# Kernel optimization log

Measured on AMD Instinct MI355X. Metric: run time of the kernel, lower is better.

Reference implementation:

```python
import jax, jax.numpy as jnp
import numpy as np

N_NODES = 100000
N_EDGES = 1600000
N_GRAPHS = 512
IN_DIM, HID, GOUT, SCAL = 256, 128, 64, 2


def setup_inputs() -> dict:
    key = jax.random.key(0)
    ks = jax.random.split(key, 12)
    x = jax.random.normal(ks[0], (N_NODES, IN_DIM), dtype=jnp.float32)
    edge_index = jax.random.randint(ks[1], (2, N_EDGES), 0, N_NODES, dtype=jnp.int64)
    batch = jnp.sort(jax.random.randint(ks[2], (N_NODES,), 0, N_GRAPHS, dtype=jnp.int64))
    scalars = jax.random.normal(ks[3], (N_GRAPHS, SCAL), dtype=jnp.float32)
    def lin(k, fan_in, fan_out):
        s = 1.0 / np.sqrt(fan_in)
        kw, kb = jax.random.split(k)
        W = jax.random.uniform(kw, (fan_in, fan_out), minval=-s, maxval=s, dtype=jnp.float32)
        b = jax.random.uniform(kb, (fan_out,), minval=-s, maxval=s, dtype=jnp.float32)
        return W, b
    W1, b1 = lin(ks[4], IN_DIM, HID)
    W2, b2 = lin(ks[5], HID, GOUT)
    W3, b3 = lin(ks[6], GOUT + SCAL, HID)
    W4, b4 = lin(ks[7], HID, 1)
    return {"x": x, "edge_index": edge_index, "batch": batch, "scalars": scalars,
            "W1": W1, "b1": b1, "W2": W2, "b2": b2,
            "W3": W3, "b3": b3, "W4": W4, "b4": b4}


def gcn_conv(x, W, b, src, dst, num_nodes):
    # PyG GCNConv: h = x @ W; add self-loops; norm = d^-1/2[src] * d^-1/2[dst]
    # with deg = in-degree (on dst) + 1 (self-loop); scatter-add into dst.
    h = x @ W  # [N, F]
    deg = jax.ops.segment_sum(jnp.ones((src.shape[0],), h.dtype), dst,
                              num_segments=num_nodes) + 1.0
    dinv = jax.lax.rsqrt(deg)  # [N]
    norm = dinv[src] * dinv[dst]  # [E]
    agg = jax.ops.segment_sum(h[src] * norm[:, None], dst, num_segments=num_nodes)
    agg = agg + h * (dinv * dinv)[:, None]  # self-loop contribution
    return agg + b


def global_mean_pool(x, batch, num_graphs):
    s = jax.ops.segment_sum(x, batch, num_segments=num_graphs)
    cnt = jax.ops.segment_sum(jnp.ones((x.shape[0],), x.dtype), batch,
                              num_segments=num_graphs)
    return s / jnp.maximum(cnt, 1.0)[:, None]


def reference(x, edge_index, batch, scalars, W1, b1, W2, b2, W3, b3, W4, b4):
    src, dst = edge_index[0], edge_index[1]
    h = jax.nn.relu(gcn_conv(x, W1, b1, src, dst, N_NODES))
    h = gcn_conv(h, W2, b2, src, dst, N_NODES)
    emb = global_mean_pool(h, batch, N_GRAPHS)  # [G, GOUT]
    combined = jnp.concatenate([emb, scalars], axis=1)  # [G, GOUT+SCAL]
    out = jax.nn.sigmoid(jax.nn.relu(combined @ W3 + b3) @ W4 + b4)
    return out.reshape(-1, 1)
```

## Files before the change

### kernel.cpp

```cpp
#include <hip/hip_runtime.h>

#define NN 100000
#define NE 1600000
#define NG 512
#define NPARTS 500
#define PW 200
#define NCHUNKS 128
#define CE 12500
#define NCNT (NPARTS * NCHUNKS)

typedef unsigned int uint;
typedef unsigned short ushort;
typedef __bf16 bf16x8 __attribute__((ext_vector_type(8)));
typedef float f32x4 __attribute__((ext_vector_type(4)));

__device__ inline uint f2bf2(float a, float b) {
  uint ua = __float_as_uint(a), ub = __float_as_uint(b);
  ua += 0x7fff + ((ua >> 16) & 1);
  ub += 0x7fff + ((ub >> 16) & 1);
  return (ua >> 16) | (ub & 0xffff0000u);
}
__device__ inline ushort f2bf(float f) {
  uint u = __float_as_uint(f);
  u += 0x7fff + ((u >> 16) & 1);
  return (ushort)(u >> 16);
}
__device__ inline float2 bf2f(uint v) {
  float2 r;
  r.x = __uint_as_float(v << 16);
  r.y = __uint_as_float(v & 0xffff0000u);
  return r;
}
__device__ inline uint relu2(uint u) {
  uint lo = (u & 0x8000u) ? 0u : (u & 0xFFFFu);
  uint hi = (u & 0x80000000u) ? 0u : (u & 0xFFFF0000u);
  return lo | hi;
}

__global__ __launch_bounds__(256) void transpose_w2(const float* __restrict__ W1, uint* __restrict__ w1t,
                                                    const float* __restrict__ W2, uint* __restrict__ w2t) {
  __shared__ float col[256];
  int b = blockIdx.x, k = threadIdx.x;
  const float* W; uint* Wt; int K, N, n;
  if (b < 128) { W = W1; Wt = w1t; K = 256; N = 128; n = b; }
  else         { W = W2; Wt = w2t; K = 128; N = 64;  n = b - 128; }
  if (k < K) col[k] = W[(size_t)k * N + n];
  __syncthreads();
  if (k < K / 2) Wt[(size_t)n * (K / 2) + k] = f2bf2(col[2 * k], col[2 * k + 1]);
}

__global__ __launch_bounds__(256) void bucket_count(const int* __restrict__ dst,
                                                    int* __restrict__ cnt) {
  __shared__ int h[NPARTS];
  int t = threadIdx.x, c = blockIdx.x;
  for (int i = t; i < NPARTS; i += 256) h[i] = 0;
  __syncthreads();
  int beg = c * CE;
  for (int j = t; j < CE; j += 256) atomicAdd(&h[dst[beg + j] / PW], 1);
  __syncthreads();
  for (int i = t; i < NPARTS; i += 256) cnt[i * NCHUNKS + c] = h[i];
}

__global__ void scan1(const int* __restrict__ in, int* __restrict__ out,
                      int* __restrict__ bsum, int n) {
  __shared__ int s[256];
  int t = threadIdx.x;
  int i = blockIdx.x * 256 + t;
  int v = (i < n) ? in[i] : 0;
  s[t] = v;
  __syncthreads();
  for (int off = 1; off < 256; off <<= 1) {
    int add = (t >= off) ? s[t - off] : 0;
    __syncthreads();
    s[t] += add;
    __syncthreads();
  }
  if (i < n) out[i] = s[t] - v;
  if (t == 255) bsum[blockIdx.x] = s[255];
}

__global__ void scan2(int* __restrict__ bsum, int nb) {
  __shared__ int s[512];
  int t = threadIdx.x;
  int v = (t < nb) ? bsum[t] : 0;
  s[t] = v;
  __syncthreads();
  for (int off = 1; off < 512; off <<= 1) {
    int add = (t >= off) ? s[t - off] : 0;
    __syncthreads();
    s[t] += add;
    __syncthreads();
  }
  if (t < nb) bsum[t] = s[t] - v;
}

__global__ void scan3(int* __restrict__ out, const int* __restrict__ bsum, int n) {
  int i = blockIdx.x * 256 + threadIdx.x;
  if (i < n) out[i] += bsum[blockIdx.x];
}

__global__ __launch_bounds__(256) void bucket_scatter(const int* __restrict__ src,
                                                      const int* __restrict__ dst,
                                                      const int* __restrict__ off,
                                                      uint* __restrict__ pk) {
  __shared__ int cur[NPARTS];
  int t = threadIdx.x, c = blockIdx.x;
  for (int i = t; i < NPARTS; i += 256) cur[i] = off[i * NCHUNKS + c];
  __syncthreads();
  int beg = c * CE;
  for (int j = t; j < CE; j += 256) {
    int d = dst[beg + j];
    int p = d / PW;
    int pos = atomicAdd(&cur[p], 1);
    pk[pos] = (uint)src[beg + j] | ((uint)(d - p * PW) << 17);
  }
}

__global__ __launch_bounds__(256) void csr_finalize(const uint* __restrict__ pk,
                                                    const int* __restrict__ off,
                                                    int* __restrict__ row_off,
                                                    float* __restrict__ dinv,
                                                    int* __restrict__ csr) {
  __shared__ int hist[PW];
  __shared__ int cur[PW];
  __shared__ int s[256];
  int p = blockIdx.x, t = threadIdx.x;
  int base = off[p * NCHUNKS];
  int endp = (p == NPARTS - 1) ? NE : off[(p + 1) * NCHUNKS];
  if (t < PW) hist[t] = 0;
  __syncthreads();
  for (int j = base + t; j < endp; j += 256) atomicAdd(&hist[pk[j] >> 17], 1);
  __syncthreads();
  int v = (t < PW) ? hist[t] : 0;
  s[t] = v;
  __syncthreads();
  for (int o = 1; o < 256; o <<= 1) {
    int add = (t >= o) ? s[t - o] : 0;
    __syncthreads();
    s[t] += add;
    __syncthreads();
  }
  if (t < PW) {
    int excl = base + (s[t] - v);
    int node = p * PW + t;
    row_off[node] = excl;
    dinv[node]    = rsqrtf((float)v + 1.0f);
    cur[t] = excl;
  }
  if (p == NPARTS - 1 && t == 0) row_off[NN] = NE;
  __syncthreads();
  for (int j = base + t; j < endp; j += 256) {
    uint e = pk[j];
    int pos = atomicAdd(&cur[e >> 17], 1);
    csr[pos] = (int)(e & 0x1FFFFu);
  }
}

template<int BM, int BN, int WM, int A_BF16, int RELU>
__global__ __launch_bounds__(256) void mfma_gemm(const void* __restrict__ Av,
                                                 const uint* __restrict__ Bt,
                                                 const float* __restrict__ dinv,
                                                 ushort* __restrict__ Cb,
                                                 int M, int K, int N) {
  constexpr int BK = 32;
  constexpr int AU = BM * BK / 8;
  constexpr int BU = BN * BK / 8;
  __shared__ __align__(16) char smem[BM * BK * 2 + BN * BK * 2];
  char* Asm = smem;
  char* Bsm = smem + BM * BK * 2;

  const int tid  = threadIdx.x;
  const int wid  = tid >> 6;
  const int lane = tid & 63;
  const int wm   = wid % WM;
  const int wn   = wid / WM;
  const int blockRow = blockIdx.x * BM;
  const int l15  = lane & 15;
  const int lk   = lane >> 4;

  f32x4 acc[4][4];
#pragma unroll
  for (int i = 0; i < 4; ++i)
#pragma unroll
    for (int j = 0; j < 4; ++j) acc[i][j] = (f32x4){0.f, 0.f, 0.f, 0.f};

  for (int kk = 0; kk < K; kk += BK) {
#pragma unroll
    for (int i = 0; i < AU / 256; ++i) {
      int u = tid + i * 256;
      int row = u >> 2, oct = u & 3;
      int grow = blockRow + row;
      uint4 v = make_uint4(0, 0, 0, 0);
      if (grow < M) {
        if (A_BF16) {
          const uint* A = (const uint*)Av;
          v = *reinterpret_cast<const uint4*>(A + (size_t)grow * (K / 2) + (kk >> 1) + oct * 4);
          if (RELU) { v.x = relu2(v.x); v.y = relu2(v.y); v.z = relu2(v.z); v.w = relu2(v.w); }
        } else {
          const float* A = (const float*)Av;
          const float4* ptr = reinterpret_cast<const float4*>(A + (size_t)grow * K + kk + oct * 8);
          float4 f0 = ptr[0], f1 = ptr[1];
          v.x = f2bf2(f0.x, f0.y); v.y = f2bf2(f0.z, f0.w);
          v.z = f2bf2(f1.x, f1.y); v.w = f2bf2(f1.z, f1.w);
        }
      }
      int byte = (row * 64 + oct * 16) ^ ((row & 7) << 4);
      *reinterpret_cast<uint4*>(Asm + byte) = v;
    }
#pragma unroll
    for (int i = 0; i < BU / 256; ++i) {
      int u = tid + i * 256;
      int n = u >> 2, oct = u & 3;
      uint4 v = *reinterpret_cast<const uint4*>(Bt + (size_t)n * (K / 2) + (kk >> 1) + oct * 4);
      int byte = (n * 64 + oct * 16) ^ ((n & 7) << 4);
      *reinterpret_cast<uint4*>(Bsm + byte) = v;
    }
    __syncthreads();

    bf16x8 af[4], bfr[4];
#pragma unroll
    for (int mt = 0; mt < 4; ++mt) {
      int row = wm * 64 + mt * 16 + l15;
      int byte = (row * 64 + (lk << 4)) ^ ((row & 7) << 4);
      af[mt] = __builtin_bit_cast(bf16x8, *reinterpret_cast<uint4*>(Asm + byte));
    }
#pragma unroll
    for (int nt = 0; nt < 4; ++nt) {
      int n = wn * 64 + nt * 16 + l15;
      int byte = (n * 64 + (lk << 4)) ^ ((n & 7) << 4);
      bfr[nt] = __builtin_bit_cast(bf16x8, *reinterpret_cast<uint4*>(Bsm + byte));
    }
#pragma unroll
    for (int mt = 0; mt < 4; ++mt)
#pragma unroll
      for (int nt = 0; nt < 4; ++nt)
        acc[mt][nt] = __builtin_amdgcn_mfma_f32_16x16x32_bf16(af[mt], bfr[nt], acc[mt][nt], 0, 0, 0);
    __syncthreads();
  }

#pragma unroll
  for (int mt = 0; mt < 4; ++mt) {
    int rbase = blockRow + wm * 64 + mt * 16 + lk * 4;
#pragma unroll
    for (int j = 0; j < 4; ++j) {
      int grow = rbase + j;
      if (grow < M) {
        float d = dinv[grow];
#pragma unroll
        for (int nt = 0; nt < 4; ++nt) {
          int gcol = wn * 64 + nt * 16 + l15;
          Cb[(size_t)grow * N + gcol] = f2bf(acc[mt][nt][j] * d);
        }
      }
    }
  }
}

__global__ __launch_bounds__(256) void agg_csr_f128_v2(const uint4* __restrict__ hs,
                                                       const float* __restrict__ dinv,
                                                       const float* __restrict__ bias,
                                                       const int* __restrict__ row_off,
                                                       const int* __restrict__ csr,
                                                       uint4* __restrict__ outb, int N) {
  int node = blockIdx.x * 4 + (threadIdx.x >> 6);
  if (node >= N) return;
  int lane = threadIdx.x & 63;
  int sl = lane >> 4;
  int c4 = lane & 15;
  int beg = row_off[node], end = row_off[node + 1];
  float a0=0,a1=0,a2=0,a3=0,a4=0,a5=0,a6=0,a7=0;
  int j = beg;
  for (; j + 16 <= end; j += 16) {
    int s0 = csr[j + sl];
    int s1 = csr[j + 4 + sl];
    int s2 = csr[j + 8 + sl];
    int s3 = csr[j + 12 + sl];
    uint4 v0 = hs[(size_t)s0 * 16 + c4];
    uint4 v1 = hs[(size_t)s1 * 16 + c4];
    uint4 v2 = hs[(size_t)s2 * 16 + c4];
    uint4 v3 = hs[(size_t)s3 * 16 + c4];
    float2 f;
    f = bf2f(v0.x); a0+=f.x; a1+=f.y;  f = bf2f(v0.y); a2+=f.x; a3+=f.y;
    f = bf2f(v0.z); a4+=f.x; a5+=f.y;  f = bf2f(v0.w); a6+=f.x; a7+=f.y;
    f = bf2f(v1.x); a0+=f.x; a1+=f.y;  f = bf2f(v1.y); a2+=f.x; a3+=f.y;
    f = bf2f(v1.z); a4+=f.x; a5+=f.y;  f = bf2f(v1.w); a6+=f.x; a7+=f.y;
    f = bf2f(v2.x); a0+=f.x; a1+=f.y;  f = bf2f(v2.y); a2+=f.x; a3+=f.y;
    f = bf2f(v2.z); a4+=f.x; a5+=f.y;  f = bf2f(v2.w); a6+=f.x; a7+=f.y;
    f = bf2f(v3.x); a0+=f.x; a1+=f.y;  f = bf2f(v3.y); a2+=f.x; a3+=f.y;
    f = bf2f(v3.z); a4+=f.x; a5+=f.y;  f = bf2f(v3.w); a6+=f.x; a7+=f.y;
  }
  for (; j + 4 <= end; j += 4) {
    int s0 = csr[j + sl];
    uint4 v0 = hs[(size_t)s0 * 16 + c4];
    float2 f;
    f = bf2f(v0.x); a0+=f.x; a1+=f.y;  f = bf2f(v0.y); a2+=f.x; a3+=f.y;
    f = bf2f(v0.z); a4+=f.x; a5+=f.y;  f = bf2f(v0.w); a6+=f.x; a7+=f.y;
  }
  if (j + sl < end) {
    int s0 = csr[j + sl];
    uint4 v0 = hs[(size_t)s0 * 16 + c4];
    float2 f;
    f = bf2f(v0.x); a0+=f.x; a1+=f.y;  f = bf2f(v0.y); a2+=f.x; a3+=f.y;
    f = bf2f(v0.z); a4+=f.x; a5+=f.y;  f = bf2f(v0.w); a6+=f.x; a7+=f.y;
  }
  a0 += __shfl_xor(a0, 16); a1 += __shfl_xor(a1, 16); a2 += __shfl_xor(a2, 16); a3 += __shfl_xor(a3, 16);
  a4 += __shfl_xor(a4, 16); a5 += __shfl_xor(a5, 16); a6 += __shfl_xor(a6, 16); a7 += __shfl_xor(a7, 16);
  a0 += __shfl_xor(a0, 32); a1 += __shfl_xor(a1, 32); a2 += __shfl_xor(a2, 32); a3 += __shfl_xor(a3, 32);
  a4 += __shfl_xor(a4, 32); a5 += __shfl_xor(a5, 32); a6 += __shfl_xor(a6, 32); a7 += __shfl_xor(a7, 32);
  if (sl == 0) {
    uint4 v = hs[(size_t)node * 16 + c4];
    float2 f;
    f = bf2f(v.x); a0+=f.x; a1+=f.y;  f = bf2f(v.y); a2+=f.x; a3+=f.y;
    f = bf2f(v.z); a4+=f.x; a5+=f.y;  f = bf2f(v.w); a6+=f.x; a7+=f.y;
    float d = dinv[node];
    const float4* bp = reinterpret_cast<const float4*>(bias);
    float4 b0 = bp[c4 * 2], b1 = bp[c4 * 2 + 1];
    uint4 o;
    o.x = f2bf2(fmaf(a0, d, b0.x), fmaf(a1, d, b0.y));
    o.y = f2bf2(fmaf(a2, d, b0.z), fmaf(a3, d, b0.w));
    o.z = f2bf2(fmaf(a4, d, b1.x), fmaf(a5, d, b1.y));
    o.w = f2bf2(fmaf(a6, d, b1.z), fmaf(a7, d, b1.w));
    outb[(size_t)node * 16 + c4] = o;
  }
}

__global__ __launch_bounds__(256) void agg_csr_f64_v2(const uint4* __restrict__ hs,
                                                      const float* __restrict__ dinv,
                                                      const int* __restrict__ row_off,
                                                      const int* __restrict__ csr,
                                                      float* __restrict__ out, int N) {
  int node = blockIdx.x * 4 + (threadIdx.x >> 6);
  if (node >= N) return;
  int lane = threadIdx.x & 63;
  int sl = lane >> 3;
  int c4 = lane & 7;
  int beg = row_off[node], end = row_off[node + 1];
  float a0=0,a1=0,a2=0,a3=0,a4=0,a5=0,a6=0,a7=0;
  int j = beg;
  for (; j + 16 <= end; j += 16) {
    int s0 = csr[j + sl];
    int s1 = csr[j + 8 + sl];
    uint4 v0 = hs[(size_t)s0 * 8 + c4];
    uint4 v1 = hs[(size_t)s1 * 8 + c4];
    float2 f;
    f = bf2f(v0.x); a0+=f.x; a1+=f.y;  f = bf2f(v0.y); a2+=f.x; a3+=f.y;
    f = bf2f(v0.z); a4+=f.x; a5+=f.y;  f = bf2f(v0.w); a6+=f.x; a7+=f.y;
    f = bf2f(v1.x); a0+=f.x; a1+=f.y;  f = bf2f(v1.y); a2+=f.x; a3+=f.y;
    f = bf2f(v1.z); a4+=f.x; a5+=f.y;  f = bf2f(v1.w); a6+=f.x; a7+=f.y;
  }
  for (; j + 8 <= end; j += 8) {
    int s0 = csr[j + sl];
    uint4 v0 = hs[(size_t)s0 * 8 + c4];
    float2 f;
    f = bf2f(v0.x); a0+=f.x; a1+=f.y;  f = bf2f(v0.y); a2+=f.x; a3+=f.y;
    f = bf2f(v0.z); a4+=f.x; a5+=f.y;  f = bf2f(v0.w); a6+=f.x; a7+=f.y;
  }
  if (j + sl < end) {
    int s0 = csr[j + sl];
    uint4 v0 = hs[(size_t)s0 * 8 + c4];
    float2 f;
    f = bf2f(v0.x); a0+=f.x; a1+=f.y;  f = bf2f(v0.y); a2+=f.x; a3+=f.y;
    f = bf2f(v0.z); a4+=f.x; a5+=f.y;  f = bf2f(v0.w); a6+=f.x; a7+=f.y;
  }
  a0 += __shfl_xor(a0, 8);  a1 += __shfl_xor(a1, 8);  a2 += __shfl_xor(a2, 8);  a3 += __shfl_xor(a3, 8);
  a4 += __shfl_xor(a4, 8);  a5 += __shfl_xor(a5, 8);  a6 += __shfl_xor(a6, 8);  a7 += __shfl_xor(a7, 8);
  a0 += __shfl_xor(a0, 16); a1 += __shfl_xor(a1, 16); a2 += __shfl_xor(a2, 16); a3 += __shfl_xor(a3, 16);
  a4 += __shfl_xor(a4, 16); a5 += __shfl_xor(a5, 16); a6 += __shfl_xor(a6, 16); a7 += __shfl_xor(a7, 16);
  a0 += __shfl_xor(a0, 32); a1 += __shfl_xor(a1, 32); a2 += __shfl_xor(a2, 32); a3 += __shfl_xor(a3, 32);
  a4 += __shfl_xor(a4, 32); a5 += __shfl_xor(a5, 32); a6 += __shfl_xor(a6, 32); a7 += __shfl_xor(a7, 32);
  if (sl == 0) {
    uint4 v = hs[(size_t)node * 8 + c4];
    float2 f;
    f = bf2f(v.x); a0+=f.x; a1+=f.y;  f = bf2f(v.y); a2+=f.x; a3+=f.y;
    f = bf2f(v.z); a4+=f.x; a5+=f.y;  f = bf2f(v.w); a6+=f.x; a7+=f.y;
    float d = dinv[node];
    float4 o0 = make_float4(a0 * d, a1 * d, a2 * d, a3 * d);
    float4 o1 = make_float4(a4 * d, a5 * d, a6 * d, a7 * d);
    float4* op = reinterpret_cast<float4*>(out + (size_t)node * 64 + c4 * 8);
    op[0] = o0;
    op[1] = o1;
  }
}

__global__ __launch_bounds__(256) void pool_graph(const float* __restrict__ h,
                                                  const int* __restrict__ batch,
                                                  const float* __restrict__ scalars,
                                                  float* __restrict__ emb66, int N) {
  int g = blockIdx.x;
  int t = threadIdx.x;
  int col = t & 63, rr = t >> 6;
  __shared__ int range[2];
  __shared__ float part[4][64];
  if (t < 2) {
    int target = g + t;
    int lo = 0, hi = N;
    while (lo < hi) { int mid = (lo + hi) >> 1; if (batch[mid] < target) lo = mid + 1; else hi = mid; }
    range[t] = lo;
  }
  __syncthreads();
  int beg = range[0], end = range[1];
  float s = 0.f;
  for (int i = beg + rr; i < end; i += 4) s += h[(size_t)i * 64 + col];
  part[rr][col] = s;
  __syncthreads();
  if (rr == 0) {
    float tot = (part[0][col] + part[1][col]) + (part[2][col] + part[3][col]);
    emb66[g * 66 + col] = tot / fmaxf((float)(end - beg), 1.f);
  } else if (t >= 64 && t < 66) {
    emb66[g * 66 + t] = scalars[g * 2 + (t - 64)];
  }
}

__global__ __launch_bounds__(128) void graph_mlp3(const float* __restrict__ emb66,
                                                  const float* __restrict__ b2,
                                                  const float* __restrict__ W3,
                                                  const float* __restrict__ b3,
                                                  const float* __restrict__ W4,
                                                  const float* __restrict__ b4,
                                                  float* __restrict__ out) {
  int g = blockIdx.x;
  int t = threadIdx.x;
  __shared__ float comb[66];
  __shared__ float part[2];
  if (t < 64)      comb[t] = emb66[g * 66 + t] + b2[t];
  else if (t < 66) comb[t] = emb66[g * 66 + t];
  __syncthreads();
  float h = b3[t];
#pragma unroll
  for (int k = 0; k < 66; ++k) h += comb[k] * W3[k * 128 + t];
  h = fmaxf(h, 0.f);
  float p = h * W4[t];
#pragma unroll
  for (int off = 32; off > 0; off >>= 1) p += __shfl_down(p, off);
  if ((t & 63) == 0) part[t >> 6] = p;
  __syncthreads();
  if (t == 0) {
    float s = part[0] + part[1] + b4[0];
    out[g] = 1.f / (1.f + expf(-s));
  }
}

extern "C" void kernel_launch(void* const* d_in, const int* in_sizes, int n_in,
                              void* d_out, int out_size, void* d_ws, size_t ws_size,
                              hipStream_t stream) {
  const float* x       = (const float*)d_in[0];
  const int*   ei      = (const int*)d_in[1];
  const int*   src     = ei;
  const int*   dstp    = ei + NE;
  const int*   batch   = (const int*)d_in[2];
  const float* scalars = (const float*)d_in[3];
  const float* W1 = (const float*)d_in[4];  const float* b1 = (const float*)d_in[5];
  const float* W2 = (const float*)d_in[6];  const float* b2 = (const float*)d_in[7];
  const float* W3 = (const float*)d_in[8];  const float* b3 = (const float*)d_in[9];
  const float* W4 = (const float*)d_in[10]; const float* b4 = (const float*)d_in[11];
  float* out = (float*)d_out;

  uint*  ws      = (uint*)d_ws;
  uint*  hsb     = ws;
  uint*  agg1b   = ws + 6400000;
  float* dinv    = (float*)(ws + 12800000);
  int*   row_off = (int*)(dinv + NN);
  int*   csr     = row_off + NN + 1;
  uint*  pk      = (uint*)(csr + NE);
  int*   cnt     = (int*)(pk + NE);
  int*   bsum    = cnt + NCNT;
  uint*  w1t     = (uint*)(bsum + 512);
  uint*  w2t     = w1t + 128 * 128;
  float* emb66   = (float*)(w2t + 64 * 64);

  bucket_count<<<NCHUNKS, 256, 0, stream>>>(dstp, cnt);
  scan1<<<(NCNT + 255) / 256, 256, 0, stream>>>(cnt, cnt, bsum, NCNT);
  scan2<<<1, 512, 0, stream>>>(bsum, (NCNT + 255) / 256);
  scan3<<<(NCNT + 255) / 256, 256, 0, stream>>>(cnt, bsum, NCNT);
  bucket_scatter<<<NCHUNKS, 256, 0, stream>>>(src, dstp, cnt, pk);
  csr_finalize<<<NPARTS, 256, 0, stream>>>(pk, cnt, row_off, dinv, csr);

  transpose_w2<<<192, 256, 0, stream>>>(W1, w1t, W2, w2t);

  mfma_gemm<128, 128, 2, 0, 0><<<(NN + 127) / 128, 256, 0, stream>>>(
      x, w1t, dinv, (ushort*)hsb, NN, 256, 128);
  agg_csr_f128_v2<<<(NN + 3) / 4, 256, 0, stream>>>((const uint4*)hsb, dinv, b1,
                                                    row_off, csr, (uint4*)agg1b, NN);

  mfma_gemm<256, 64, 4, 1, 1><<<(NN + 255) / 256, 256, 0, stream>>>(
      agg1b, w2t, dinv, (ushort*)hsb, NN, 128, 64);
  agg_csr_f64_v2<<<(NN + 3) / 4, 256, 0, stream>>>((const uint4*)hsb, dinv,
                                                   row_off, csr, (float*)agg1b, NN);

  pool_graph<<<NG, 256, 0, stream>>>((const float*)agg1b, batch, scalars, emb66, NN);
  graph_mlp3<<<NG, 128, 0, stream>>>(emb66, b2, W3, b3, W4, b4, out);
}
```

Measured before the change: 253.8 us.

## Replace tiled GEMM with direct-from-global A loads and whole-B LDS residency

The K-looped GEMM that staged both A and B tiles through shared memory is replaced by a kernel that loads all of the transposed weight matrix into LDS once. It then streams A fragments straight from global memory into MFMA registers, with no per-k-step barriers. Block tiles shrink to 64 or 128 rows, which gives more blocks and more parallelism but less reuse of each A fragment across waves. The workspace is reordered so the weight buffers sit at the front and the CSR array is aligned.

```diff
diff --git a/kernel.cpp b/kernel.cpp
--- a/kernel.cpp
+++ b/kernel.cpp
@@ -156,91 +156,75 @@
   }
 }
 
-template<int BM, int BN, int WM, int A_BF16, int RELU>
-__global__ __launch_bounds__(256) void mfma_gemm(const void* __restrict__ Av,
-                                                 const uint* __restrict__ Bt,
-                                                 const float* __restrict__ dinv,
-                                                 ushort* __restrict__ Cb,
-                                                 int M, int K, int N) {
-  constexpr int BK = 32;
-  constexpr int AU = BM * BK / 8;
-  constexpr int BU = BN * BK / 8;
-  __shared__ __align__(16) char smem[BM * BK * 2 + BN * BK * 2];
-  char* Asm = smem;
-  char* Bsm = smem + BM * BK * 2;
-
+template<int K, int N, int WM, int WN, int A_BF16, int RELU>
+__global__ __launch_bounds__(256) void gemm_direct(const void* __restrict__ Av,
+                                                   const uint* __restrict__ Bt,
+                                                   const float* __restrict__ dinv,
+                                                   ushort* __restrict__ Cb, int M) {
+  __shared__ __align__(16) char bsm[N * K * 2];
   const int tid  = threadIdx.x;
   const int wid  = tid >> 6;
   const int lane = tid & 63;
   const int wm   = wid % WM;
   const int wn   = wid / WM;
-  const int blockRow = blockIdx.x * BM;
   const int l15  = lane & 15;
   const int lk   = lane >> 4;
-
-  f32x4 acc[4][4];
-#pragma unroll
-  for (int i = 0; i < 4; ++i)
+  const int blockRow = blockIdx.x * (WM * 32);
+
+  constexpr int UPR = K / 8;
+  constexpr int TOT = N * K / 8;
+#pragma unroll
+  for (int i0 = 0; i0 < TOT; i0 += 256) {
+    int i = i0 + tid;
+    uint4 v = reinterpret_cast<const uint4*>(Bt)[i];
+    int n = i / UPR, c = i % UPR;
+    int byte = (n * (K * 2) + c * 16) ^ ((n & 7) << 4);
+    *reinterpret_cast<uint4*>(bsm + byte) = v;
+  }
+  __syncthreads();
+
+  f32x4 acc[2][4];
+#pragma unroll
+  for (int i = 0; i < 2; ++i)
 #pragma unroll
     for (int j = 0; j < 4; ++j) acc[i][j] = (f32x4){0.f, 0.f, 0.f, 0.f};
 
-  for (int kk = 0; kk < K; kk += BK) {
-#pragma unroll
-    for (int i = 0; i < AU / 256; ++i) {
-      int u = tid + i * 256;
-      int row = u >> 2, oct = u & 3;
-      int grow = blockRow + row;
-      uint4 v = make_uint4(0, 0, 0, 0);
-      if (grow < M) {
-        if (A_BF16) {
-          const uint* A = (const uint*)Av;
-          v = *reinterpret_cast<const uint4*>(A + (size_t)grow * (K / 2) + (kk >> 1) + oct * 4);
-          if (RELU) { v.x = relu2(v.x); v.y = relu2(v.y); v.z = relu2(v.z); v.w = relu2(v.w); }
-        } else {
-          const float* A = (const float*)Av;
-          const float4* ptr = reinterpret_cast<const float4*>(A + (size_t)grow * K + kk + oct * 8);
-          float4 f0 = ptr[0], f1 = ptr[1];
-          v.x = f2bf2(f0.x, f0.y); v.y = f2bf2(f0.z, f0.w);
-          v.z = f2bf2(f1.x, f1.y); v.w = f2bf2(f1.z, f1.w);
-        }
+#pragma unroll
+  for (int kk = 0; kk < K / 32; ++kk) {
+    bf16x8 af[2], bfr[4];
+#pragma unroll
+    for (int mt = 0; mt < 2; ++mt) {
+      int grow = blockRow + wm * 32 + mt * 16 + l15;
+      int row = grow < M ? grow : M - 1;
+      if (A_BF16) {
+        uint4 va = *reinterpret_cast<const uint4*>((const uint*)Av + (size_t)row * (K / 2) + kk * 16 + lk * 4);
+        if (RELU) { va.x = relu2(va.x); va.y = relu2(va.y); va.z = relu2(va.z); va.w = relu2(va.w); }
+        af[mt] = __builtin_bit_cast(bf16x8, va);
+      } else {
+        const float4* p = reinterpret_cast<const float4*>((const float*)Av + (size_t)row * K + kk * 32 + lk * 8);
+        float4 f0 = p[0], f1 = p[1];
+        uint4 va;
+        va.x = f2bf2(f0.x, f0.y); va.y = f2bf2(f0.z, f0.w);
+        va.z = f2bf2(f1.x, f1.y); va.w = f2bf2(f1.z, f1.w);
+        af[mt] = __builtin_bit_cast(bf16x8, va);
       }
-      int byte = (row * 64 + oct * 16) ^ ((row & 7) << 4);
-      *reinterpret_cast<uint4*>(Asm + byte) = v;
-    }
-#pragma unroll
-    for (int i = 0; i < BU / 256; ++i) {
-      int u = tid + i * 256;
-      int n = u >> 2, oct = u & 3;
-      uint4 v = *reinterpret_cast<const uint4*>(Bt + (size_t)n * (K / 2) + (kk >> 1) + oct * 4);
-      int byte = (n * 64 + oct * 16) ^ ((n & 7) << 4);
-      *reinterpret_cast<uint4*>(Bsm + byte) = v;
-    }
-    __syncthreads();
-
-    bf16x8 af[4], bfr[4];
-#pragma unroll
-    for (int mt = 0; mt < 4; ++mt) {
-      int row = wm * 64 + mt * 16 + l15;
-      int byte = (row * 64 + (lk << 4)) ^ ((row & 7) << 4);
-      af[mt] = __builtin_bit_cast(bf16x8, *reinterpret_cast<uint4*>(Asm + byte));
     }
 #pragma unroll
     for (int nt = 0; nt < 4; ++nt) {
       int n = wn * 64 + nt * 16 + l15;
-      int byte = (n * 64 + (lk << 4)) ^ ((n & 7) << 4);
-      bfr[nt] = __builtin_bit_cast(bf16x8, *reinterpret_cast<uint4*>(Bsm + byte));
+      int byte = (n * (K * 2) + kk * 64 + lk * 16) ^ ((n & 7) << 4);
+      bfr[nt] = __builtin_bit_cast(bf16x8, *reinterpret_cast<uint4*>(bsm + byte));
     }
 #pragma unroll
-    for (int mt = 0; mt < 4; ++mt)
+    for (int mt = 0; mt < 2; ++mt)
 #pragma unroll
       for (int nt = 0; nt < 4; ++nt)
         acc[mt][nt] = __builtin_amdgcn_mfma_f32_16x16x32_bf16(af[mt], bfr[nt], acc[mt][nt], 0, 0, 0);
-    __syncthreads();
-  }
-
-#pragma unroll
-  for (int mt = 0; mt < 4; ++mt) {
-    int rbase = blockRow + wm * 64 + mt * 16 + lk * 4;
+  }
+
+#pragma unroll
+  for (int mt = 0; mt < 2; ++mt) {
+    int rbase = blockRow + wm * 32 + mt * 16 + lk * 4;
 #pragma unroll
     for (int j = 0; j < 4; ++j) {
       int grow = rbase + j;
@@ -456,17 +440,17 @@
   float* out = (float*)d_out;
 
   uint*  ws      = (uint*)d_ws;
-  uint*  hsb     = ws;
-  uint*  agg1b   = ws + 6400000;
-  float* dinv    = (float*)(ws + 12800000);
+  uint*  w1t     = ws;
+  uint*  w2t     = ws + 16384;
+  uint*  hsb     = ws + 20480;
+  uint*  agg1b   = hsb + 6400000;
+  float* dinv    = (float*)(agg1b + 6400000);
   int*   row_off = (int*)(dinv + NN);
-  int*   csr     = row_off + NN + 1;
+  int*   csr     = row_off + NN + 4;
   uint*  pk      = (uint*)(csr + NE);
   int*   cnt     = (int*)(pk + NE);
   int*   bsum    = cnt + NCNT;
-  uint*  w1t     = (uint*)(bsum + 512);
-  uint*  w2t     = w1t + 128 * 128;
-  float* emb66   = (float*)(w2t + 64 * 64);
+  float* emb66   = (float*)(bsum + 512);
 
   bucket_count<<<NCHUNKS, 256, 0, stream>>>(dstp, cnt);
   scan1<<<(NCNT + 255) / 256, 256, 0, stream>>>(cnt, cnt, bsum, NCNT);
@@ -477,13 +461,13 @@
 
   transpose_w2<<<192, 256, 0, stream>>>(W1, w1t, W2, w2t);
 
-  mfma_gemm<128, 128, 2, 0, 0><<<(NN + 127) / 128, 256, 0, stream>>>(
-      x, w1t, dinv, (ushort*)hsb, NN, 256, 128);
+  gemm_direct<256, 128, 2, 2, 0, 0><<<(NN + 63) / 64, 256, 0, stream>>>(
+      x, w1t, dinv, (ushort*)hsb, NN);
   agg_csr_f128_v2<<<(NN + 3) / 4, 256, 0, stream>>>((const uint4*)hsb, dinv, b1,
                                                     row_off, csr, (uint4*)agg1b, NN);
 
-  mfma_gemm<256, 64, 4, 1, 1><<<(NN + 255) / 256, 256, 0, stream>>>(
-      agg1b, w2t, dinv, (ushort*)hsb, NN, 128, 64);
+  gemm_direct<128, 64, 4, 1, 1, 1><<<(NN + 127) / 128, 256, 0, stream>>>(
+      agg1b, w2t, dinv, (ushort*)hsb, NN);
   agg_csr_f64_v2<<<(NN + 3) / 4, 256, 0, stream>>>((const uint4*)hsb, dinv,
                                                    row_off, csr, (float*)agg1b, NN);
 
```

After: 251.3 us. Within noise of the previous version (-1.0%).
